# Performance work log

Measured on AMD Instinct MI355X. Metric: run time of the kernel, lower is better.

The kernel has to match this reference:

```python
import jax, jax.numpy as jnp
import numpy as np

MAX_CHILD = 64  # max trie branching factor (padding width for per-row child windows)


def setup_inputs() -> dict:
    key = jax.random.key(0)
    B, D, V, N = 1024, 1024, 32000, 200000
    k1, k2, k3, k4 = jax.random.split(key, 4)
    x = jax.random.normal(k1, (B, D), dtype=jnp.float32)
    weight = jax.random.normal(k2, (V, D), dtype=jnp.float32) * 0.02
    bias = jax.random.normal(k3, (V,), dtype=jnp.float32) * 0.02
    # Build a consistent CompactCSRTrie: offsets [N+1], tokens/child_nodes [E]
    rng = np.random.default_rng(0)
    deg = rng.integers(1, MAX_CHILD + 1, size=N)
    offsets = np.zeros(N + 1, dtype=np.int32)
    offsets[1:] = np.cumsum(deg)
    E = int(offsets[-1])
    tokens = rng.integers(0, V, size=E).astype(np.int32)
    child_nodes = rng.integers(0, N, size=E).astype(np.int32)
    cur_node = jax.random.randint(k4, (B,), 0, N, dtype=jnp.int32)
    return {
        "x": x,
        "weight": weight,
        "bias": bias,
        "cur_node": cur_node,
        "offsets": jnp.asarray(offsets),
        "tokens": jnp.asarray(tokens),
        "child_nodes": jnp.asarray(child_nodes),
        "step": 1,
    }


def reference(x, weight, bias, cur_node, offsets, tokens, child_nodes, step):
    # Dense GEMM part of the fused kernel: logits = x @ W^T + b  -> [B, V]
    logits = jnp.einsum("bd,vd->bv", x, weight) + bias
    B, V = logits.shape

    # CSR trie traversal: per row, the children of cur_node are
    # tokens[offsets[cur]:offsets[cur+1]] (valid next tokens) and
    # child_nodes[...] (next trie nodes). Gather a padded MAX_CHILD window.
    start = offsets[cur_node]                              # [B]
    deg = offsets[cur_node + 1] - start                    # [B]
    pos = jnp.arange(MAX_CHILD, dtype=start.dtype)         # [C]
    idx = jnp.minimum(start[:, None] + pos[None, :], tokens.shape[0] - 1)  # [B, C]
    valid = pos[None, :] < deg[:, None]                    # [B, C] bool

    tok = tokens[idx]                                      # [B, C] valid token columns
    child = child_nodes[idx]                               # [B, C] next trie nodes

    # Validity masking: only valid child tokens keep their logit, rest -> -inf
    rows = jnp.arange(B)[:, None]
    mask = jnp.zeros((B, V), dtype=bool).at[rows, tok].max(valid)
    masked_logits = jnp.where(mask, logits, -jnp.inf)

    next_nodes = jnp.where(valid, child, -1)               # [B, C], -1 padded
    valid_idxs = jnp.where(valid, tok, -1)                 # [B, C], -1 padded
    return next_nodes, valid_idxs, masked_logits
```

## Files before the change

kernel.cpp:

```cpp
#include <hip/hip_runtime.h>
#include <math.h>

#define B_ 1024
#define D_ 1024
#define V_ 32000
#define MAXC 64
#define HDR (2 * B_ * MAXC)
#define LOGF4 ((B_ * V_) / 4)
#define NGATHER 1024
#define NFILL 2048
#define FILL_F4 4096

#define NEG_FILL (-3.0e38f)

typedef float vfloat4 __attribute__((ext_vector_type(4)));

__global__ __launch_bounds__(256, 8) void fill_gather_kernel(
    const float* __restrict__ x,
    const float* __restrict__ weight,
    const float* __restrict__ bias,
    const int* __restrict__ cur_node,
    const int* __restrict__ offsets,
    const int* __restrict__ tokens,
    float* __restrict__ out)
{
    const int bid = blockIdx.x;
    const int tid = threadIdx.x;

    if (bid >= NGATHER) {
        vfloat4* ml4 = reinterpret_cast<vfloat4*>(out + HDR);
        const vfloat4 sent = {NEG_FILL, NEG_FILL, NEG_FILL, NEG_FILL};
        const int base = (bid - NGATHER) * FILL_F4 + tid;
        #pragma unroll
        for (int j = 0; j < FILL_F4 / 256; ++j) {
            const int i = base + j * 256;
            if (i < LOGF4)
                __builtin_nontemporal_store(sent, &ml4[i]);
        }
        return;
    }

    const int b    = bid;
    const int wave = tid >> 6;
    const int lane = tid & 63;

    const int cur = cur_node[b];
    const int start = offsets[cur];
    int deg = offsets[cur + 1] - start;
    if (deg > MAXC) deg = MAXC;

    const float4* x4 = reinterpret_cast<const float4*>(x + (size_t)b * D_);
    float4 xv[4];
    #pragma unroll
    for (int k = 0; k < 4; ++k)
        xv[k] = x4[k * 64 + lane];

    const int sbase = wave * 16;
    int cnt = deg - sbase;
    if (cnt < 0) cnt = 0;
    if (cnt > 16) cnt = 16;

    int tok = 0;
    float bv = 0.0f;
    if (lane < 16 && sbase + lane < deg) {
        tok = tokens[start + sbase + lane];
        bv = bias[tok];
    }

    float myval = 0.0f;
    float4 wA[4], wB[4];
    if (cnt > 0) {
        const int t0 = __shfl(tok, 0);
        const float4* w4 = reinterpret_cast<const float4*>(weight + (size_t)t0 * D_);
        #pragma unroll
        for (int k = 0; k < 4; ++k) wA[k] = w4[k * 64 + lane];
    }
    int i = 0;
    while (i < cnt) {
        if (i + 1 < cnt) {
            const int t = __shfl(tok, i + 1);
            const float4* w4 = reinterpret_cast<const float4*>(weight + (size_t)t * D_);
            #pragma unroll
            for (int k = 0; k < 4; ++k) wB[k] = w4[k * 64 + lane];
        }
        {
            float acc = 0.0f;
            #pragma unroll
            for (int k = 0; k < 4; ++k)
                acc += wA[k].x * xv[k].x + wA[k].y * xv[k].y +
                       wA[k].z * xv[k].z + wA[k].w * xv[k].w;
            #pragma unroll
            for (int off = 32; off > 0; off >>= 1)
                acc += __shfl_xor(acc, off);
            if (lane == i) myval = acc + bv;
        }
        ++i;
        if (i >= cnt) break;
        if (i + 1 < cnt) {
            const int t = __shfl(tok, i + 1);
            const float4* w4 = reinterpret_cast<const float4*>(weight + (size_t)t * D_);
            #pragma unroll
            for (int k = 0; k < 4; ++k) wA[k] = w4[k * 64 + lane];
        }
        {
            float acc = 0.0f;
            #pragma unroll
            for (int k = 0; k < 4; ++k)
                acc += wB[k].x * xv[k].x + wB[k].y * xv[k].y +
                       wB[k].z * xv[k].z + wB[k].w * xv[k].w;
            #pragma unroll
            for (int off = 32; off > 0; off >>= 1)
                acc += __shfl_xor(acc, off);
            if (lane == i) myval = acc + bv;
        }
        ++i;
    }

    if (lane < 16 && sbase + lane < deg)
        out[b * MAXC + sbase + lane] = myval;
}

__global__ __launch_bounds__(256) void scatter_kernel(
    const int* __restrict__ cur_node,
    const int* __restrict__ offsets,
    const int* __restrict__ tokens,
    const int* __restrict__ child_nodes,
    float* __restrict__ out)
{
    const int gid = blockIdx.x * 256 + threadIdx.x;
    const int b = gid >> 6;
    const int c = gid & (MAXC - 1);

    const int cur = cur_node[b];
    const int start = offsets[cur];
    int deg = offsets[cur + 1] - start;
    if (deg > MAXC) deg = MAXC;

    float nn = -1.0f, vi = -1.0f;
    if (c < deg) {
        const int e = start + c;
        const int tok = tokens[e];
        const float val = out[gid];
        out[HDR + (size_t)b * V_ + tok] = val;
        nn = (float)child_nodes[e];
        vi = (float)tok;
    }
    out[gid] = nn;
    out[(size_t)B_ * MAXC + gid] = vi;
}

extern "C" void kernel_launch(void* const* d_in, const int* in_sizes, int n_in,
                              void* d_out, int out_size, void* d_ws, size_t ws_size,
                              hipStream_t stream) {
    const float* x           = (const float*)d_in[0];
    const float* weight      = (const float*)d_in[1];
    const float* bias        = (const float*)d_in[2];
    const int*   cur_node    = (const int*)d_in[3];
    const int*   offsets     = (const int*)d_in[4];
    const int*   tokens      = (const int*)d_in[5];
    const int*   child_nodes = (const int*)d_in[6];

    float* out = (float*)d_out;

    fill_gather_kernel<<<NGATHER + NFILL, 256, 0, stream>>>(
        x, weight, bias, cur_node, offsets, tokens, out);
    scatter_kernel<<<(B_ * MAXC) / 256, 256, 0, stream>>>(
        cur_node, offsets, tokens, child_nodes, out);
}
```

Measured before the change: 57.31 us.

## Fuse fill, gather-dot and scatter into one per-row kernel

Merges the two kernels into a single launch. Each block fills its own masked-logits row with the sentinel, computes the dot products for the valid children, stages them in shared memory, and scatters them into the row after a block barrier. Next-node and valid-index outputs are also written in the same block. This removes the second launch and the round trip of the intermediate values through global memory. In exchange, the fill is now interleaved with the gather work inside each block instead of running in separate blocks, and launch bounds drop to 4 blocks per SM.

Measured after the change: 51.77 us. 9.7% less time.

```diff
diff --git a/kernel.cpp b/kernel.cpp
--- a/kernel.cpp
+++ b/kernel.cpp
@@ -5,42 +5,28 @@
 #define D_ 1024
 #define V_ 32000
 #define MAXC 64
-#define HDR (2 * B_ * MAXC)
-#define LOGF4 ((B_ * V_) / 4)
-#define NGATHER 1024
-#define NFILL 2048
-#define FILL_F4 4096
 
 #define NEG_FILL (-3.0e38f)
 
 typedef float vfloat4 __attribute__((ext_vector_type(4)));
 
-__global__ __launch_bounds__(256, 8) void fill_gather_kernel(
+__global__ __launch_bounds__(256, 4) void constrained_linear_kernel(
     const float* __restrict__ x,
     const float* __restrict__ weight,
     const float* __restrict__ bias,
     const int* __restrict__ cur_node,
     const int* __restrict__ offsets,
     const int* __restrict__ tokens,
-    float* __restrict__ out)
+    const int* __restrict__ child_nodes,
+    float* __restrict__ next_nodes,
+    float* __restrict__ valid_idxs,
+    float* __restrict__ masked_logits)
 {
-    const int bid = blockIdx.x;
-    const int tid = threadIdx.x;
+    __shared__ int   ltok[MAXC];
+    __shared__ float lval[MAXC];
 
-    if (bid >= NGATHER) {
-        vfloat4* ml4 = reinterpret_cast<vfloat4*>(out + HDR);
-        const vfloat4 sent = {NEG_FILL, NEG_FILL, NEG_FILL, NEG_FILL};
-        const int base = (bid - NGATHER) * FILL_F4 + tid;
-        #pragma unroll
-        for (int j = 0; j < FILL_F4 / 256; ++j) {
-            const int i = base + j * 256;
-            if (i < LOGF4)
-                __builtin_nontemporal_store(sent, &ml4[i]);
-        }
-        return;
-    }
-
-    const int b    = bid;
+    const int b    = blockIdx.x;
+    const int tid  = threadIdx.x;
     const int wave = tid >> 6;
     const int lane = tid & 63;
 
@@ -49,12 +35,6 @@
     int deg = offsets[cur + 1] - start;
     if (deg > MAXC) deg = MAXC;
 
-    const float4* x4 = reinterpret_cast<const float4*>(x + (size_t)b * D_);
-    float4 xv[4];
-    #pragma unroll
-    for (int k = 0; k < 4; ++k)
-        xv[k] = x4[k * 64 + lane];
-
     const int sbase = wave * 16;
     int cnt = deg - sbase;
     if (cnt < 0) cnt = 0;
@@ -62,12 +42,23 @@
 
     int tok = 0;
     float bv = 0.0f;
-    if (lane < 16 && sbase + lane < deg) {
-        tok = tokens[start + sbase + lane];
-        bv = bias[tok];
+    if (lane < 16) {
+        const int s = sbase + lane;
+        if (s < deg) {
+            tok = tokens[start + s];
+            bv = bias[tok];
+            ltok[s] = tok;
+        } else {
+            ltok[s] = -1;
+        }
     }
 
-    float myval = 0.0f;
+    const float4* x4 = reinterpret_cast<const float4*>(x + (size_t)b * D_);
+    float4 xv[4];
+    #pragma unroll
+    for (int k = 0; k < 4; ++k)
+        xv[k] = x4[k * 64 + lane];
+
     float4 wA[4], wB[4];
     if (cnt > 0) {
         const int t0 = __shfl(tok, 0);
@@ -75,6 +66,25 @@
         #pragma unroll
         for (int k = 0; k < 4; ++k) wA[k] = w4[k * 64 + lane];
     }
+
+    if (tid < MAXC) {
+        float nn = -1.0f, vi = -1.0f;
+        if (tid < deg) {
+            const int e = start + tid;
+            nn = (float)child_nodes[e];
+            vi = (float)tokens[e];
+        }
+        next_nodes[b * MAXC + tid] = nn;
+        valid_idxs[b * MAXC + tid] = vi;
+    }
+
+    float* ml_row = masked_logits + (size_t)b * V_;
+    vfloat4* ml4 = reinterpret_cast<vfloat4*>(ml_row);
+    const vfloat4 sent = {NEG_FILL, NEG_FILL, NEG_FILL, NEG_FILL};
+    #pragma unroll 4
+    for (int i = tid; i < V_ / 4; i += 256)
+        __builtin_nontemporal_store(sent, &ml4[i]);
+
     int i = 0;
     while (i < cnt) {
         if (i + 1 < cnt) {
@@ -92,7 +102,7 @@
             #pragma unroll
             for (int off = 32; off > 0; off >>= 1)
                 acc += __shfl_xor(acc, off);
-            if (lane == i) myval = acc + bv;
+            if (lane == i) lval[sbase + i] = acc + bv;
         }
         ++i;
         if (i >= cnt) break;
@@ -111,42 +121,18 @@
             #pragma unroll
             for (int off = 32; off > 0; off >>= 1)
                 acc += __shfl_xor(acc, off);
-            if (lane == i) myval = acc + bv;
+            if (lane == i) lval[sbase + i] = acc + bv;
         }
         ++i;
     }
 
-    if (lane < 16 && sbase + lane < deg)
-        out[b * MAXC + sbase + lane] = myval;
-}
+    __syncthreads();
 
-__global__ __launch_bounds__(256) void scatter_kernel(
-    const int* __restrict__ cur_node,
-    const int* __restrict__ offsets,
-    const int* __restrict__ tokens,
-    const int* __restrict__ child_nodes,
-    float* __restrict__ out)
-{
-    const int gid = blockIdx.x * 256 + threadIdx.x;
-    const int b = gid >> 6;
-    const int c = gid & (MAXC - 1);
-
-    const int cur = cur_node[b];
-    const int start = offsets[cur];
-    int deg = offsets[cur + 1] - start;
-    if (deg > MAXC) deg = MAXC;
-
-    float nn = -1.0f, vi = -1.0f;
-    if (c < deg) {
-        const int e = start + c;
-        const int tok = tokens[e];
-        const float val = out[gid];
-        out[HDR + (size_t)b * V_ + tok] = val;
-        nn = (float)child_nodes[e];
-        vi = (float)tok;
+    if (tid < MAXC) {
+        const int t = ltok[tid];
+        if (t >= 0)
+            ml_row[t] = lval[tid];
     }
-    out[gid] = nn;
-    out[(size_t)B_ * MAXC + gid] = vi;
 }
 
 extern "C" void kernel_launch(void* const* d_in, const int* in_sizes, int n_in,
@@ -161,9 +147,11 @@
     const int*   child_nodes = (const int*)d_in[6];
 
     float* out = (float*)d_out;
+    float* next_nodes    = out;
+    float* valid_idxs    = out + (size_t)B_ * MAXC;
+    float* masked_logits = out + 2 * (size_t)B_ * MAXC;
 
-    fill_gather_kernel<<<NGATHER + NFILL, 256, 0, stream>>>(
-        x, weight, bias, cur_node, offsets, tokens, out);
-    scatter_kernel<<<(B_ * MAXC) / 256, 256, 0, stream>>>(
-        cur_node, offsets, tokens, child_nodes, out);
+    constrained_linear_kernel<<<B_, 256, 0, stream>>>(
+        x, weight, bias, cur_node, offsets, tokens, child_nodes,
+        next_nodes, valid_idxs, masked_logits);
 }
```
